# Performance work log

Hardware: AMD Instinct MI355X
Metric: run time of the kernel (lower is better)

## Reference

```python
import jax, jax.numpy as jnp
import numpy as np

N_NODE, N_NET, E = 100000, 20000, 200000
H_NODE, H_NET, H_PIN = 64, 32, 16
O_NODE, O_NET = 32, 64


def setup_inputs() -> dict:
    key = jax.random.key(0)
    ks = jax.random.split(key, 8)
    return {
        'node_feat': jax.random.normal(ks[0], (N_NODE, H_NODE), jnp.float32),
        'net_feat': jax.random.normal(ks[1], (N_NET, H_NET), jnp.float32),
        'pin_feat': jax.random.normal(ks[2], (E, H_PIN), jnp.float32),
        'edge_node': jax.random.randint(ks[3], (E,), 0, N_NODE, jnp.int32),
        'edge_net': jax.random.randint(ks[4], (E,), 0, N_NET, jnp.int32),
        'W1': jax.random.normal(ks[5], (H_NODE, O_NET), jnp.float32) * 0.05,
        'b1': jnp.zeros((O_NET,), jnp.float32),
        'W2': jax.random.normal(ks[6], (H_PIN, H_NET * O_NODE), jnp.float32) * 0.05,
        'b2': jnp.zeros((H_NET * O_NODE,), jnp.float32),
        'b_nn': jnp.zeros((O_NODE,), jnp.float32),
    }


def reference(node_feat, net_feat, pin_feat, edge_node, edge_net, W1, b1, W2, b2, b_nn):
    ones = jnp.ones((E,), node_feat.dtype)
    # ---- relation 'pins': node -> net, DGL GraphConv with norm='both' ----
    out_deg = jnp.clip(jax.ops.segment_sum(ones, edge_node, num_segments=N_NODE), 1.0)  # src out-degree
    in_deg = jnp.clip(jax.ops.segment_sum(ones, edge_net, num_segments=N_NET), 1.0)     # dst in-degree
    src = node_feat * jax.lax.rsqrt(out_deg)[:, None]                                   # [N_node, H_node]
    agg = jax.ops.segment_sum(src[edge_node], edge_net, num_segments=N_NET)             # [N_net, H_node]
    net_out = (agg * jax.lax.rsqrt(in_deg)[:, None]) @ W1 + b1                           # [N_net, O_net]
    # ---- relation 'pinned': net -> node, DGL NNConv (mean aggregator) ----
    We = (pin_feat @ W2 + b2).reshape(E, H_NET, O_NODE)                                  # per-edge weight matrix
    msg = jnp.einsum('ei,eio->eo', net_feat[edge_net], We)                               # [E, O_node]
    node_deg = jnp.clip(jax.ops.segment_sum(ones, edge_node, num_segments=N_NODE), 1.0)
    node_out = jax.ops.segment_sum(msg, edge_node, num_segments=N_NODE) / node_deg[:, None] + b_nn
    return node_out, net_out
```

## Files before the change

kernel.cpp:

```cpp
#include <hip/hip_runtime.h>
#include <hip/hip_bf16.h>

#define N_NODE 100000
#define N_NET  20000
#define NE     200000
#define H_NODE 64
#define H_NET  32
#define H_PIN  16
#define O_NODE 32
#define O_NET  64
#define CSR_STRIDE 64


#define OFF_NETCNT  400000
#define OFF_CSR     480000
#define OFF_Z       10720000
#define OFF_C       31200000
#define ZERO_BYTES  480000

static __device__ __forceinline__ unsigned short f2bf(float f) {
    unsigned int u = __float_as_uint(f);
    u += 0x7fff + ((u >> 16) & 1);
    return (unsigned short)(u >> 16);
}
static __device__ __forceinline__ float bf2f(unsigned short h) {
    return __uint_as_float(((unsigned int)h) << 16);
}

#define BLD_EDGE_BLKS 782
#define BLD_Z_BLKS    1250
#define BLD_INIT_BLKS 3125
#define ZNPB 16

__global__ void k_build(const int* __restrict__ en, const int* __restrict__ em,
                        int* __restrict__ node_deg, int* __restrict__ net_cnt,
                        int2* __restrict__ csr,
                        const float* __restrict__ net_feat,
                        const float* __restrict__ W2, const float* __restrict__ b2,
                        unsigned short* __restrict__ Zb, float* __restrict__ C,
                        const float* __restrict__ b_nn,
                        float* __restrict__ out_node) {
    int t = threadIdx.x, b = blockIdx.x;
    if (b < BLD_EDGE_BLKS) {
        int e = b * 256 + t;
        if (e < NE) {
            int v = en[e], n = em[e];
            atomicAdd(&node_deg[v], 1);
            int slot = atomicAdd(&net_cnt[n], 1);
            if (slot < CSR_STRIDE) csr[n * CSR_STRIDE + slot] = make_int2(e, v);
        }
        return;
    }
    if (b < BLD_EDGE_BLKS + BLD_Z_BLKS) {
        __shared__ float sy[ZNPB][H_NET];
        int base = (b - BLD_EDGE_BLKS) * ZNPB;
        for (int idx = t; idx < ZNPB * H_NET; idx += 256)
            sy[idx >> 5][idx & 31] = net_feat[(base + (idx >> 5)) * H_NET + (idx & 31)];
        __syncthreads();
        int o = t & 31, k4 = (t >> 5) & 3, rep = t >> 7;
        const float* w2p = W2 + (k4 * 4) * 1024 + o;
        float4 acc[8];
#pragma unroll
        for (int g = 0; g < 8; g++) acc[g] = make_float4(0.f, 0.f, 0.f, 0.f);
#pragma unroll 4
        for (int i = 0; i < H_NET; i++) {
            float w0 = w2p[0 * 1024 + i * 32];
            float w1 = w2p[1 * 1024 + i * 32];
            float w2v = w2p[2 * 1024 + i * 32];
            float w3 = w2p[3 * 1024 + i * 32];
#pragma unroll
            for (int g = 0; g < 8; g++) {
                float y = sy[rep * 8 + g][i];
                acc[g].x += w0 * y; acc[g].y += w1 * y;
                acc[g].z += w2v * y; acc[g].w += w3 * y;
            }
        }
#pragma unroll
        for (int g = 0; g < 8; g++) {
            int n = base + rep * 8 + g;
            ushort4 uz;
            uz.x = f2bf(acc[g].x); uz.y = f2bf(acc[g].y);
            uz.z = f2bf(acc[g].z); uz.w = f2bf(acc[g].w);
            *(ushort4*)&Zb[(size_t)n * 512 + o * 16 + k4 * 4] = uz;
        }
#pragma unroll
        for (int r = 0; r < 2; r++) {
            int idx = t + r * 256;
            int g = idx >> 5, oo = idx & 31;
            float a = 0.f;
#pragma unroll
            for (int i = 0; i < H_NET; i++) a += sy[g][i] * b2[i * 32 + oo];
            C[(base + g) * 32 + oo] = a;
        }
        return;
    }
    int idx = (b - BLD_EDGE_BLKS - BLD_Z_BLKS) * 256 + t;
    ((float4*)out_node)[idx] = ((const float4*)b_nn)[idx & 7];
}

__global__ void k_net(const float* __restrict__ node_feat,
                      const int* __restrict__ node_deg,
                      const int* __restrict__ net_cnt,
                      const int2* __restrict__ csr,
                      const float* __restrict__ W1,
                      const float* __restrict__ b1,
                      const unsigned short* __restrict__ Zb,
                      const float* __restrict__ Cg,
                      const float* __restrict__ pin_feat,
                      float* __restrict__ out_net, float* __restrict__ out_node) {
    __shared__ float  spin[4][32][16];
    __shared__ float4 srow4[4][16];
    int t = threadIdx.x;
    int w = t >> 6, l = t & 63;
    int n = blockIdx.x * 4 + w;
    int beg = n * CSR_STRIDE, deg = net_cnt[n];
    int o = l & 31;
    int half = l >> 5;
    int q = l >> 4, f = l & 15;

    float z[16];
    {
        const uint4* zp = (const uint4*)&Zb[(size_t)n * 512 + o * 16];
        uint4 za = zp[0], zb = zp[1];
        unsigned int uu[8] = {za.x, za.y, za.z, za.w, zb.x, zb.y, zb.z, zb.w};
#pragma unroll
        for (int i = 0; i < 8; i++) {
            z[2 * i]     = bf2f((unsigned short)(uu[i] & 0xffffu));
            z[2 * i + 1] = bf2f((unsigned short)(uu[i] >> 16));
        }
    }
    float c = Cg[n * 32 + o];

    const float4* nf4 = (const float4*)node_feat;
    const float4* pf4 = (const float4*)pin_feat;

    float4 acc4 = make_float4(0.f, 0.f, 0.f, 0.f);

    for (int j0 = 0; j0 < deg; j0 += 32) {
        int cnt = deg - j0; if (cnt > 32) cnt = 32;
        int vj = 0, ej = 0; float sj = 0.f;
        if (l < cnt) {
            int2 ev = csr[beg + j0 + l];
            ej = ev.x; vj = ev.y;
            float dv = (float)node_deg[vj]; if (dv < 1.f) dv = 1.f;
            sj = rsqrtf(dv);
        }
        {
            int jj = l >> 2;
            int src = (jj < cnt) ? jj : cnt - 1;
            int e = __shfl(ej, src);
            float4 pv = pf4[(size_t)e * 4 + (l & 3)];
            ((float4*)&spin[w][jj][0])[l & 3] = pv;
        }
        if (cnt > 16) {
            int jj = 16 + (l >> 2);
            int src = (jj < cnt) ? jj : cnt - 1;
            int e = __shfl(ej, src);
            float4 pv = pf4[(size_t)e * 4 + (l & 3)];
            ((float4*)&spin[w][jj][0])[l & 3] = pv;
        }
        {
            int vv[4]; float ss[4];
#pragma unroll
            for (int r = 0; r < 4; r++) {
                int jj = r * 4 + q;
                int src = (jj < cnt) ? jj : cnt - 1;
                vv[r] = __shfl(vj, src);
                float sv = __shfl(sj, src);
                ss[r] = (jj < cnt) ? sv : 0.f;
            }
            float4 xx[4];
#pragma unroll
            for (int r = 0; r < 4; r++) xx[r] = nf4[(size_t)vv[r] * 16 + f];
#pragma unroll
            for (int r = 0; r < 4; r++) {
                acc4.x += xx[r].x * ss[r]; acc4.y += xx[r].y * ss[r];
                acc4.z += xx[r].z * ss[r]; acc4.w += xx[r].w * ss[r];
            }
        }
        if (cnt > 16) {
            int vv[4]; float ss[4];
#pragma unroll
            for (int r = 0; r < 4; r++) {
                int jj = 16 + r * 4 + q;
                int src = (jj < cnt) ? jj : cnt - 1;
                vv[r] = __shfl(vj, src);
                float sv = __shfl(sj, src);
                ss[r] = (jj < cnt) ? sv : 0.f;
            }
            float4 xx[4];
#pragma unroll
            for (int r = 0; r < 4; r++) xx[r] = nf4[(size_t)vv[r] * 16 + f];
#pragma unroll
            for (int r = 0; r < 4; r++) {
                acc4.x += xx[r].x * ss[r]; acc4.y += xx[r].y * ss[r];
                acc4.z += xx[r].z * ss[r]; acc4.w += xx[r].w * ss[r];
            }
        }
        for (int jj = 0; jj < cnt; jj += 2) {
            int je = jj + half;
            int src = (je < cnt) ? je : cnt - 1;
            int v = __shfl(vj, src);
            float sv = __shfl(sj, src);
            float inv = sv * sv;
            const float4* pr = (const float4*)&spin[w][src][0];
            float m = c;
#pragma unroll
            for (int k4 = 0; k4 < 4; k4++) {
                float4 pv = pr[k4];
                m += pv.x * z[k4 * 4 + 0] + pv.y * z[k4 * 4 + 1]
                   + pv.z * z[k4 * 4 + 2] + pv.w * z[k4 * 4 + 3];
            }
            if (je < cnt) atomicAdd(&out_node[(size_t)v * O_NODE + o], m * inv);
        }
    }
    acc4.x += __shfl_xor(acc4.x, 16); acc4.y += __shfl_xor(acc4.y, 16);
    acc4.z += __shfl_xor(acc4.z, 16); acc4.w += __shfl_xor(acc4.w, 16);
    acc4.x += __shfl_xor(acc4.x, 32); acc4.y += __shfl_xor(acc4.y, 32);
    acc4.z += __shfl_xor(acc4.z, 32); acc4.w += __shfl_xor(acc4.w, 32);
    float dn = (deg < 1) ? 1.f : (float)deg;
    float rs = rsqrtf(dn);
    if (l < 16)
        srow4[w][l] = make_float4(acc4.x * rs, acc4.y * rs, acc4.z * rs, acc4.w * rs);
    __syncthreads();
    {
        const float* a = (const float*)&srow4[w][0];
        float oacc = b1[l];
#pragma unroll 16
        for (int h = 0; h < H_NODE; h++) oacc += a[h] * W1[h * O_NET + l];
        out_net[n * O_NET + l] = oacc;
    }
}

extern "C" void kernel_launch(void* const* d_in, const int* in_sizes, int n_in,
                              void* d_out, int out_size, void* d_ws, size_t ws_size,
                              hipStream_t stream) {
    const float* node_feat = (const float*)d_in[0];
    const float* net_feat  = (const float*)d_in[1];
    const float* pin_feat  = (const float*)d_in[2];
    const int*   edge_node = (const int*)d_in[3];
    const int*   edge_net  = (const int*)d_in[4];
    const float* W1        = (const float*)d_in[5];
    const float* b1        = (const float*)d_in[6];
    const float* W2        = (const float*)d_in[7];
    const float* b2        = (const float*)d_in[8];
    const float* b_nn      = (const float*)d_in[9];

    float* out_node = (float*)d_out;
    float* out_net  = out_node + (size_t)N_NODE * O_NODE;

    char* ws = (char*)d_ws;
    int*            node_deg = (int*)ws;
    int*            net_cnt  = (int*)(ws + OFF_NETCNT);
    int2*           csr      = (int2*)(ws + OFF_CSR);
    unsigned short* Zb       = (unsigned short*)(ws + OFF_Z);
    float*          C        = (float*)(ws + OFF_C);

    (void)hipMemsetAsync(ws, 0, ZERO_BYTES, stream);

    k_build<<<BLD_EDGE_BLKS + BLD_Z_BLKS + BLD_INIT_BLKS, 256, 0, stream>>>(
        edge_node, edge_net, node_deg, net_cnt, csr,
        net_feat, W2, b2, Zb, C, b_nn, out_node);

    k_net<<<N_NET / 4, 256, 0, stream>>>(
        node_feat, node_deg, net_cnt, csr,
        W1, b1, Zb, C, pin_feat, out_net, out_node);
}
```

Measured before the change: 163.7 us.

## Merge build and net kernels into one persistent cooperative kernel with grid sync

Combines the graph-build/Z-precompute kernel and the per-net aggregation kernel into a single cooperative persistent kernel separated by a grid-wide barrier, with a fallback to the two-kernel path. Aims to remove the inter-kernel launch gap and tail. Adds per-call host occupancy queries, restricts grid size to resident blocks (less latency hiding via oversubscription), and drops the block barrier before the W1 projection, relying on intra-wave LDS ordering.

```diff
diff --git a/kernel.cpp b/kernel.cpp
--- a/kernel.cpp
+++ b/kernel.cpp
@@ -1,5 +1,8 @@
 #include <hip/hip_runtime.h>
 #include <hip/hip_bf16.h>
+#include <hip/hip_cooperative_groups.h>
+
+namespace cg = cooperative_groups;
 
 #define N_NODE 100000
 #define N_NET  20000
@@ -11,6 +14,8 @@
 #define O_NET  64
 #define CSR_STRIDE 64
 
+#define ZNPB 16
+
 
 #define OFF_NETCNT  400000
 #define OFF_CSR     480000
@@ -27,10 +32,177 @@
     return __uint_as_float(((unsigned int)h) << 16);
 }
 
+
+static __device__ __forceinline__ void zc_body(int vb, int t,
+        const float* __restrict__ net_feat, const float* __restrict__ W2,
+        const float* __restrict__ b2, unsigned short* __restrict__ Zb,
+        float* __restrict__ C, float sy[ZNPB][H_NET]) {
+    int base = vb * ZNPB;
+    for (int idx = t; idx < ZNPB * H_NET; idx += 256)
+        sy[idx >> 5][idx & 31] = net_feat[(base + (idx >> 5)) * H_NET + (idx & 31)];
+    __syncthreads();
+    int o = t & 31, k4 = (t >> 5) & 3, rep = t >> 7;
+    const float* w2p = W2 + (k4 * 4) * 1024 + o;
+    float4 acc[8];
+#pragma unroll
+    for (int g = 0; g < 8; g++) acc[g] = make_float4(0.f, 0.f, 0.f, 0.f);
+#pragma unroll 4
+    for (int i = 0; i < H_NET; i++) {
+        float w0 = w2p[0 * 1024 + i * 32];
+        float w1 = w2p[1 * 1024 + i * 32];
+        float w2v = w2p[2 * 1024 + i * 32];
+        float w3 = w2p[3 * 1024 + i * 32];
+#pragma unroll
+        for (int g = 0; g < 8; g++) {
+            float y = sy[rep * 8 + g][i];
+            acc[g].x += w0 * y; acc[g].y += w1 * y;
+            acc[g].z += w2v * y; acc[g].w += w3 * y;
+        }
+    }
+#pragma unroll
+    for (int g = 0; g < 8; g++) {
+        int n = base + rep * 8 + g;
+        ushort4 uz;
+        uz.x = f2bf(acc[g].x); uz.y = f2bf(acc[g].y);
+        uz.z = f2bf(acc[g].z); uz.w = f2bf(acc[g].w);
+        *(ushort4*)&Zb[(size_t)n * 512 + o * 16 + k4 * 4] = uz;
+    }
+#pragma unroll
+    for (int r = 0; r < 2; r++) {
+        int idx = t + r * 256;
+        int g = idx >> 5, oo = idx & 31;
+        float a = 0.f;
+#pragma unroll
+        for (int i = 0; i < H_NET; i++) a += sy[g][i] * b2[i * 32 + oo];
+        C[(base + g) * 32 + oo] = a;
+    }
+}
+
+static __device__ __forceinline__ void net_body(int n, int w, int l,
+        const float* __restrict__ node_feat, const int* __restrict__ node_deg,
+        const int* __restrict__ net_cnt, const int2* __restrict__ csr,
+        const float* __restrict__ W1, const float* __restrict__ b1,
+        const unsigned short* __restrict__ Zb, const float* __restrict__ Cg,
+        const float* __restrict__ pin_feat,
+        float* __restrict__ out_net, float* __restrict__ out_node,
+        float spin[4][32][16], float4 srow4[4][16]) {
+    int beg = n * CSR_STRIDE, deg = net_cnt[n];
+    int o = l & 31, half = l >> 5, q = l >> 4, f = l & 15;
+
+    float z[16];
+    {
+        const uint4* zp = (const uint4*)&Zb[(size_t)n * 512 + o * 16];
+        uint4 za = zp[0], zb = zp[1];
+        unsigned int uu[8] = {za.x, za.y, za.z, za.w, zb.x, zb.y, zb.z, zb.w};
+#pragma unroll
+        for (int i = 0; i < 8; i++) {
+            z[2 * i]     = bf2f((unsigned short)(uu[i] & 0xffffu));
+            z[2 * i + 1] = bf2f((unsigned short)(uu[i] >> 16));
+        }
+    }
+    float c = Cg[n * 32 + o];
+    const float4* nf4 = (const float4*)node_feat;
+    const float4* pf4 = (const float4*)pin_feat;
+    float4 acc4 = make_float4(0.f, 0.f, 0.f, 0.f);
+
+    for (int j0 = 0; j0 < deg; j0 += 32) {
+        int cnt = deg - j0; if (cnt > 32) cnt = 32;
+        int vj = 0, ej = 0; float sj = 0.f;
+        if (l < cnt) {
+            int2 ev = csr[beg + j0 + l];
+            ej = ev.x; vj = ev.y;
+            float dv = (float)node_deg[vj]; if (dv < 1.f) dv = 1.f;
+            sj = rsqrtf(dv);
+        }
+        {
+            int jj = l >> 2;
+            int src = (jj < cnt) ? jj : cnt - 1;
+            int e = __shfl(ej, src);
+            float4 pv = pf4[(size_t)e * 4 + (l & 3)];
+            ((float4*)&spin[w][jj][0])[l & 3] = pv;
+        }
+        if (cnt > 16) {
+            int jj = 16 + (l >> 2);
+            int src = (jj < cnt) ? jj : cnt - 1;
+            int e = __shfl(ej, src);
+            float4 pv = pf4[(size_t)e * 4 + (l & 3)];
+            ((float4*)&spin[w][jj][0])[l & 3] = pv;
+        }
+        {
+            int vv[4]; float ss[4];
+#pragma unroll
+            for (int r = 0; r < 4; r++) {
+                int jj = r * 4 + q;
+                int src = (jj < cnt) ? jj : cnt - 1;
+                vv[r] = __shfl(vj, src);
+                float sv = __shfl(sj, src);
+                ss[r] = (jj < cnt) ? sv : 0.f;
+            }
+            float4 xx[4];
+#pragma unroll
+            for (int r = 0; r < 4; r++) xx[r] = nf4[(size_t)vv[r] * 16 + f];
+#pragma unroll
+            for (int r = 0; r < 4; r++) {
+                acc4.x += xx[r].x * ss[r]; acc4.y += xx[r].y * ss[r];
+                acc4.z += xx[r].z * ss[r]; acc4.w += xx[r].w * ss[r];
+            }
+        }
+        if (cnt > 16) {
+            int vv[4]; float ss[4];
+#pragma unroll
+            for (int r = 0; r < 4; r++) {
+                int jj = 16 + r * 4 + q;
+                int src = (jj < cnt) ? jj : cnt - 1;
+                vv[r] = __shfl(vj, src);
+                float sv = __shfl(sj, src);
+                ss[r] = (jj < cnt) ? sv : 0.f;
+            }
+            float4 xx[4];
+#pragma unroll
+            for (int r = 0; r < 4; r++) xx[r] = nf4[(size_t)vv[r] * 16 + f];
+#pragma unroll
+            for (int r = 0; r < 4; r++) {
+                acc4.x += xx[r].x * ss[r]; acc4.y += xx[r].y * ss[r];
+                acc4.z += xx[r].z * ss[r]; acc4.w += xx[r].w * ss[r];
+            }
+        }
+        for (int jj = 0; jj < cnt; jj += 2) {
+            int je = jj + half;
+            int src = (je < cnt) ? je : cnt - 1;
+            int v = __shfl(vj, src);
+            float sv = __shfl(sj, src);
+            float inv = sv * sv;
+            const float4* pr = (const float4*)&spin[w][src][0];
+            float m = c;
+#pragma unroll
+            for (int k4 = 0; k4 < 4; k4++) {
+                float4 pv = pr[k4];
+                m += pv.x * z[k4 * 4 + 0] + pv.y * z[k4 * 4 + 1]
+                   + pv.z * z[k4 * 4 + 2] + pv.w * z[k4 * 4 + 3];
+            }
+            if (je < cnt) atomicAdd(&out_node[(size_t)v * O_NODE + o], m * inv);
+        }
+    }
+    acc4.x += __shfl_xor(acc4.x, 16); acc4.y += __shfl_xor(acc4.y, 16);
+    acc4.z += __shfl_xor(acc4.z, 16); acc4.w += __shfl_xor(acc4.w, 16);
+    acc4.x += __shfl_xor(acc4.x, 32); acc4.y += __shfl_xor(acc4.y, 32);
+    acc4.z += __shfl_xor(acc4.z, 32); acc4.w += __shfl_xor(acc4.w, 32);
+    float dn = (deg < 1) ? 1.f : (float)deg;
+    float rs = rsqrtf(dn);
+    if (l < 16)
+        srow4[w][l] = make_float4(acc4.x * rs, acc4.y * rs, acc4.z * rs, acc4.w * rs);
+    {
+        const float* a = (const float*)&srow4[w][0];
+        float oacc = b1[l];
+#pragma unroll 16
+        for (int h = 0; h < H_NODE; h++) oacc += a[h] * W1[h * O_NET + l];
+        out_net[n * O_NET + l] = oacc;
+    }
+}
+
 #define BLD_EDGE_BLKS 782
 #define BLD_Z_BLKS    1250
 #define BLD_INIT_BLKS 3125
-#define ZNPB 16
 
 __global__ void k_build(const int* __restrict__ en, const int* __restrict__ em,
                         int* __restrict__ node_deg, int* __restrict__ net_cnt,
@@ -53,45 +225,7 @@
     }
     if (b < BLD_EDGE_BLKS + BLD_Z_BLKS) {
         __shared__ float sy[ZNPB][H_NET];
-        int base = (b - BLD_EDGE_BLKS) * ZNPB;
-        for (int idx = t; idx < ZNPB * H_NET; idx += 256)
-            sy[idx >> 5][idx & 31] = net_feat[(base + (idx >> 5)) * H_NET + (idx & 31)];
-        __syncthreads();
-        int o = t & 31, k4 = (t >> 5) & 3, rep = t >> 7;
-        const float* w2p = W2 + (k4 * 4) * 1024 + o;
-        float4 acc[8];
-#pragma unroll
-        for (int g = 0; g < 8; g++) acc[g] = make_float4(0.f, 0.f, 0.f, 0.f);
-#pragma unroll 4
-        for (int i = 0; i < H_NET; i++) {
-            float w0 = w2p[0 * 1024 + i * 32];
-            float w1 = w2p[1 * 1024 + i * 32];
-            float w2v = w2p[2 * 1024 + i * 32];
-            float w3 = w2p[3 * 1024 + i * 32];
-#pragma unroll
-            for (int g = 0; g < 8; g++) {
-                float y = sy[rep * 8 + g][i];
-                acc[g].x += w0 * y; acc[g].y += w1 * y;
-                acc[g].z += w2v * y; acc[g].w += w3 * y;
-            }
-        }
-#pragma unroll
-        for (int g = 0; g < 8; g++) {
-            int n = base + rep * 8 + g;
-            ushort4 uz;
-            uz.x = f2bf(acc[g].x); uz.y = f2bf(acc[g].y);
-            uz.z = f2bf(acc[g].z); uz.w = f2bf(acc[g].w);
-            *(ushort4*)&Zb[(size_t)n * 512 + o * 16 + k4 * 4] = uz;
-        }
-#pragma unroll
-        for (int r = 0; r < 2; r++) {
-            int idx = t + r * 256;
-            int g = idx >> 5, oo = idx & 31;
-            float a = 0.f;
-#pragma unroll
-            for (int i = 0; i < H_NET; i++) a += sy[g][i] * b2[i * 32 + oo];
-            C[(base + g) * 32 + oo] = a;
-        }
+        zc_body(b - BLD_EDGE_BLKS, t, net_feat, W2, b2, Zb, C, sy);
         return;
     }
     int idx = (b - BLD_EDGE_BLKS - BLD_Z_BLKS) * 256 + t;
@@ -102,8 +236,7 @@
                       const int* __restrict__ node_deg,
                       const int* __restrict__ net_cnt,
                       const int2* __restrict__ csr,
-                      const float* __restrict__ W1,
-                      const float* __restrict__ b1,
+                      const float* __restrict__ W1, const float* __restrict__ b1,
                       const unsigned short* __restrict__ Zb,
                       const float* __restrict__ Cg,
                       const float* __restrict__ pin_feat,
@@ -113,122 +246,48 @@
     int t = threadIdx.x;
     int w = t >> 6, l = t & 63;
     int n = blockIdx.x * 4 + w;
-    int beg = n * CSR_STRIDE, deg = net_cnt[n];
-    int o = l & 31;
-    int half = l >> 5;
-    int q = l >> 4, f = l & 15;
-
-    float z[16];
-    {
-        const uint4* zp = (const uint4*)&Zb[(size_t)n * 512 + o * 16];
-        uint4 za = zp[0], zb = zp[1];
-        unsigned int uu[8] = {za.x, za.y, za.z, za.w, zb.x, zb.y, zb.z, zb.w};
-#pragma unroll
-        for (int i = 0; i < 8; i++) {
-            z[2 * i]     = bf2f((unsigned short)(uu[i] & 0xffffu));
-            z[2 * i + 1] = bf2f((unsigned short)(uu[i] >> 16));
-        }
-    }
-    float c = Cg[n * 32 + o];
-
-    const float4* nf4 = (const float4*)node_feat;
-    const float4* pf4 = (const float4*)pin_feat;
-
-    float4 acc4 = make_float4(0.f, 0.f, 0.f, 0.f);
-
-    for (int j0 = 0; j0 < deg; j0 += 32) {
-        int cnt = deg - j0; if (cnt > 32) cnt = 32;
-        int vj = 0, ej = 0; float sj = 0.f;
-        if (l < cnt) {
-            int2 ev = csr[beg + j0 + l];
-            ej = ev.x; vj = ev.y;
-            float dv = (float)node_deg[vj]; if (dv < 1.f) dv = 1.f;
-            sj = rsqrtf(dv);
-        }
-        {
-            int jj = l >> 2;
-            int src = (jj < cnt) ? jj : cnt - 1;
-            int e = __shfl(ej, src);
-            float4 pv = pf4[(size_t)e * 4 + (l & 3)];
-            ((float4*)&spin[w][jj][0])[l & 3] = pv;
-        }
-        if (cnt > 16) {
-            int jj = 16 + (l >> 2);
-            int src = (jj < cnt) ? jj : cnt - 1;
-            int e = __shfl(ej, src);
-            float4 pv = pf4[(size_t)e * 4 + (l & 3)];
-            ((float4*)&spin[w][jj][0])[l & 3] = pv;
-        }
-        {
-            int vv[4]; float ss[4];
-#pragma unroll
-            for (int r = 0; r < 4; r++) {
-                int jj = r * 4 + q;
-                int src = (jj < cnt) ? jj : cnt - 1;
-                vv[r] = __shfl(vj, src);
-                float sv = __shfl(sj, src);
-                ss[r] = (jj < cnt) ? sv : 0.f;
-            }
-            float4 xx[4];
-#pragma unroll
-            for (int r = 0; r < 4; r++) xx[r] = nf4[(size_t)vv[r] * 16 + f];
-#pragma unroll
-            for (int r = 0; r < 4; r++) {
-                acc4.x += xx[r].x * ss[r]; acc4.y += xx[r].y * ss[r];
-                acc4.z += xx[r].z * ss[r]; acc4.w += xx[r].w * ss[r];
-            }
-        }
-        if (cnt > 16) {
-            int vv[4]; float ss[4];
-#pragma unroll
-            for (int r = 0; r < 4; r++) {
-                int jj = 16 + r * 4 + q;
-                int src = (jj < cnt) ? jj : cnt - 1;
-                vv[r] = __shfl(vj, src);
-                float sv = __shfl(sj, src);
-                ss[r] = (jj < cnt) ? sv : 0.f;
-            }
-            float4 xx[4];
-#pragma unroll
-            for (int r = 0; r < 4; r++) xx[r] = nf4[(size_t)vv[r] * 16 + f];
-#pragma unroll
-            for (int r = 0; r < 4; r++) {
-                acc4.x += xx[r].x * ss[r]; acc4.y += xx[r].y * ss[r];
-                acc4.z += xx[r].z * ss[r]; acc4.w += xx[r].w * ss[r];
-            }
-        }
-        for (int jj = 0; jj < cnt; jj += 2) {
-            int je = jj + half;
-            int src = (je < cnt) ? je : cnt - 1;
-            int v = __shfl(vj, src);
-            float sv = __shfl(sj, src);
-            float inv = sv * sv;
-            const float4* pr = (const float4*)&spin[w][src][0];
-            float m = c;
-#pragma unroll
-            for (int k4 = 0; k4 < 4; k4++) {
-                float4 pv = pr[k4];
-                m += pv.x * z[k4 * 4 + 0] + pv.y * z[k4 * 4 + 1]
-                   + pv.z * z[k4 * 4 + 2] + pv.w * z[k4 * 4 + 3];
-            }
-            if (je < cnt) atomicAdd(&out_node[(size_t)v * O_NODE + o], m * inv);
-        }
-    }
-    acc4.x += __shfl_xor(acc4.x, 16); acc4.y += __shfl_xor(acc4.y, 16);
-    acc4.z += __shfl_xor(acc4.z, 16); acc4.w += __shfl_xor(acc4.w, 16);
-    acc4.x += __shfl_xor(acc4.x, 32); acc4.y += __shfl_xor(acc4.y, 32);
-    acc4.z += __shfl_xor(acc4.z, 32); acc4.w += __shfl_xor(acc4.w, 32);
-    float dn = (deg < 1) ? 1.f : (float)deg;
-    float rs = rsqrtf(dn);
-    if (l < 16)
-        srow4[w][l] = make_float4(acc4.x * rs, acc4.y * rs, acc4.z * rs, acc4.w * rs);
-    __syncthreads();
-    {
-        const float* a = (const float*)&srow4[w][0];
-        float oacc = b1[l];
-#pragma unroll 16
-        for (int h = 0; h < H_NODE; h++) oacc += a[h] * W1[h * O_NET + l];
-        out_net[n * O_NET + l] = oacc;
+    net_body(n, w, l, node_feat, node_deg, net_cnt, csr, W1, b1, Zb, Cg,
+             pin_feat, out_net, out_node, spin, srow4);
+}
+
+__global__ __launch_bounds__(256, 4)
+void k_all(const int* __restrict__ en, const int* __restrict__ em,
+           int* __restrict__ node_deg, int* __restrict__ net_cnt,
+           int2* __restrict__ csr,
+           const float* __restrict__ node_feat,
+           const float* __restrict__ net_feat,
+           const float* __restrict__ pin_feat,
+           const float* __restrict__ W1, const float* __restrict__ b1,
+           const float* __restrict__ W2, const float* __restrict__ b2,
+           const float* __restrict__ b_nn,
+           unsigned short* __restrict__ Zb, float* __restrict__ C,
+           float* __restrict__ out_net, float* __restrict__ out_node) {
+    cg::grid_group grid = cg::this_grid();
+    int t = threadIdx.x, b = blockIdx.x;
+    int nb = gridDim.x;
+    __shared__ float sy[ZNPB][H_NET];
+    __shared__ float  spin[4][32][16];
+    __shared__ float4 srow4[4][16];
+
+    for (int e = b * 256 + t; e < NE; e += nb * 256) {
+        int v = en[e], n = em[e];
+        atomicAdd(&node_deg[v], 1);
+        int slot = atomicAdd(&net_cnt[n], 1);
+        if (slot < CSR_STRIDE) csr[n * CSR_STRIDE + slot] = make_int2(e, v);
+    }
+    for (int idx = b * 256 + t; idx < N_NODE * O_NODE / 4; idx += nb * 256)
+        ((float4*)out_node)[idx] = ((const float4*)b_nn)[idx & 7];
+    for (int vb = b; vb < N_NET / ZNPB; vb += nb) {
+        __syncthreads();
+        zc_body(vb, t, net_feat, W2, b2, Zb, C, sy);
+    }
+
+    grid.sync();
+
+    int w = t >> 6, l = t & 63;
+    for (int vb = b; vb < N_NET / 4; vb += nb) {
+        net_body(vb * 4 + w, w, l, node_feat, node_deg, net_cnt, csr, W1, b1,
+                 Zb, C, pin_feat, out_net, out_node, spin, srow4);
     }
 }
 
@@ -258,11 +317,36 @@
 
     (void)hipMemsetAsync(ws, 0, ZERO_BYTES, stream);
 
-    k_build<<<BLD_EDGE_BLKS + BLD_Z_BLKS + BLD_INIT_BLKS, 256, 0, stream>>>(
-        edge_node, edge_net, node_deg, net_cnt, csr,
-        net_feat, W2, b2, Zb, C, b_nn, out_node);
-
-    k_net<<<N_NET / 4, 256, 0, stream>>>(
-        node_feat, node_deg, net_cnt, csr,
-        W1, b1, Zb, C, pin_feat, out_net, out_node);
-}
+    bool coop_done = false;
+    int dev = 0;
+    if (hipGetDevice(&dev) == hipSuccess) {
+        int coopAttr = 0;
+        (void)hipDeviceGetAttribute(&coopAttr, hipDeviceAttributeCooperativeLaunch, dev);
+        int maxPerCU = 0;
+        hipError_t qerr = hipOccupancyMaxActiveBlocksPerMultiprocessor(
+            &maxPerCU, (const void*)k_all, 256, 0);
+        if (coopAttr && qerr == hipSuccess && maxPerCU >= 1) {
+            int nblk = maxPerCU * 256;
+            if (nblk > 1024) nblk = 1024;
+            void* args[] = {
+                (void*)&edge_node, (void*)&edge_net,
+                (void*)&node_deg, (void*)&net_cnt, (void*)&csr,
+                (void*)&node_feat, (void*)&net_feat, (void*)&pin_feat,
+                (void*)&W1, (void*)&b1, (void*)&W2, (void*)&b2, (void*)&b_nn,
+                (void*)&Zb, (void*)&C, (void*)&out_net, (void*)&out_node,
+            };
+            hipError_t lerr = hipLaunchCooperativeKernel(
+                (const void*)k_all, dim3(nblk), dim3(256), args, 0, stream);
+            coop_done = (lerr == hipSuccess);
+        }
+    }
+
+    if (!coop_done) {
+        k_build<<<BLD_EDGE_BLKS + BLD_Z_BLKS + BLD_INIT_BLKS, 256, 0, stream>>>(
+            edge_node, edge_net, node_deg, net_cnt, csr,
+            net_feat, W2, b2, Zb, C, b_nn, out_node);
+        k_net<<<N_NET / 4, 256, 0, stream>>>(
+            node_feat, node_deg, net_cnt, csr,
+            W1, b1, Zb, C, pin_feat, out_net, out_node);
+    }
+}
```

After: 304.3 us. +85.9%, slower.
